# Kernel tuning notes

Hardware: AMD Instinct MI355X
Metric: run time of the kernel (lower is better)

Reference implementation:

```python
import jax, jax.numpy as jnp
import numpy as np

D_MODEL = 1024
NUM_HEADS = 16
D_K = D_MODEL // NUM_HEADS

def setup_inputs() -> dict:
    key = jax.random.key(0)
    ks = jax.random.split(key, 8)
    B, S, D = 2, 2048, D_MODEL
    scale = 1.0 / np.sqrt(D)
    return {
        "X_q": jax.random.normal(ks[0], (B, S, D), dtype=jnp.float32),
        "X_k": jax.random.normal(ks[1], (B, S, D), dtype=jnp.float32),
        "X_v": jax.random.normal(ks[2], (B, S, D), dtype=jnp.float32),
        "W_q": jax.random.normal(ks[3], (D, D), dtype=jnp.float32) * scale,
        "W_k": jax.random.normal(ks[4], (D, D), dtype=jnp.float32) * scale,
        "W_v": jax.random.normal(ks[5], (D, D), dtype=jnp.float32) * scale,
        "W_o": jax.random.normal(ks[6], (D, D), dtype=jnp.float32) * scale,
        "b_o": jnp.zeros((D,), dtype=jnp.float32),
    }

def reference(X_q, X_k, X_v, W_q, W_k, W_v, W_o, b_o):
    B, S, D = X_q.shape
    H, dk = NUM_HEADS, D_K
    # nn.Linear: x @ W.T
    Q = (X_q @ W_q.T).reshape(B, H, S, dk)  # faithful raw view, no transpose
    K = (X_k @ W_k.T).reshape(B, H, S, dk)
    V = (X_v @ W_v.T).reshape(B, H, S, dk)
    A = jnp.einsum("bhqd,bhkd->bhqk", Q, K) / np.sqrt(dk)  # [B,H,S,S]
    A = jax.nn.softmax(A, axis=-1)
    H_cat = jnp.einsum("bhqk,bhkd->bhqd", A, V).reshape(B, S, D)
    return H_cat @ W_o.T + b_o
```

## Files before the change

### kernel.cpp

```cpp
#include <hip/hip_runtime.h>

typedef __bf16 bf16;
typedef bf16 bf16x8 __attribute__((ext_vector_type(8)));
typedef bf16 bf16x4 __attribute__((ext_vector_type(4)));
typedef bf16 bf16x2 __attribute__((ext_vector_type(2)));
typedef float f32x4 __attribute__((ext_vector_type(4)));
typedef float f32x16 __attribute__((ext_vector_type(16)));
typedef int i32x4 __attribute__((ext_vector_type(4)));

#define XSZ 4194304
#define WSZ 1048576
#define KDIM 1024
#define QSCALE 0.1803368801111137f

__device__ __forceinline__ void async16(const bf16* g, bf16* l) {
  __builtin_amdgcn_global_load_lds(
      (const __attribute__((address_space(1))) unsigned int*)g,
      (__attribute__((address_space(3))) unsigned int*)l, 16, 0, 0);
}

__device__ __forceinline__ bf16x8 ld8(const bf16* p) {
  bf16x4 lo = *(const bf16x4*)p;
  bf16x4 hi = *(const bf16x4*)(p + 4);
  return __builtin_shufflevector(lo, hi, 0, 1, 2, 3, 4, 5, 6, 7);
}

__device__ __forceinline__ bf16x8 ld16(const bf16* p) {
  return __builtin_bit_cast(bf16x8, *(const i32x4*)p);
}

__device__ __forceinline__ void st8s(bf16* p, bf16x8 v) {
  *(bf16x4*)p       = __builtin_shufflevector(v, v, 0, 1, 2, 3);
  *(bf16x4*)(p + 4) = __builtin_shufflevector(v, v, 4, 5, 6, 7);
}

__device__ __forceinline__ f32x4 mfma16(bf16x8 a, bf16x8 b, f32x4 c) {
  return __builtin_amdgcn_mfma_f32_16x16x32_bf16(a, b, c, 0, 0, 0);
}
__device__ __forceinline__ f32x16 mfma32(bf16x8 a, bf16x8 b, f32x16 c) {
  return __builtin_amdgcn_mfma_f32_32x32x16_bf16(a, b, c, 0, 0, 0);
}

__device__ __forceinline__ int packbf2(float lo, float hi) {
  bf16x2 t; t[0] = (bf16)lo; t[1] = (bf16)hi;
  return __builtin_bit_cast(int, t);
}

__device__ __forceinline__ float fast_exp2(float x) {
#if __has_builtin(__builtin_amdgcn_exp2f)
  return __builtin_amdgcn_exp2f(x);
#else
  return exp2f(x);
#endif
}


__global__ __launch_bounds__(256) void cast_all(const float* __restrict__ Xq, const float* __restrict__ Xk,
                                                const float* __restrict__ Xv, const float* __restrict__ Wq,
                                                const float* __restrict__ Wk, const float* __restrict__ Wv,
                                                const float* __restrict__ Wo, bf16* __restrict__ dst) {
  size_t i = ((size_t)blockIdx.x * 256 + threadIdx.x) * 8;
  const float* src; size_t off; float scale = 1.0f;
  if (i < XSZ)                { src = Xq; off = i; }
  else if (i < 2 * (size_t)XSZ) { src = Xk; off = i - XSZ; }
  else if (i < 3 * (size_t)XSZ) { src = Xv; off = i - 2 * (size_t)XSZ; }
  else if (i < 3 * (size_t)XSZ + WSZ) { src = Wq; off = i - 3 * (size_t)XSZ; scale = QSCALE; }
  else if (i < 3 * (size_t)XSZ + 2 * (size_t)WSZ) { src = Wk; off = i - 3 * (size_t)XSZ - WSZ; }
  else if (i < 3 * (size_t)XSZ + 3 * (size_t)WSZ) { src = Wv; off = i - 3 * (size_t)XSZ - 2 * (size_t)WSZ; }
  else                        { src = Wo; off = i - 3 * (size_t)XSZ - 3 * (size_t)WSZ; }
  float4 a = *(const float4*)(src + off);
  float4 b = *(const float4*)(src + off + 4);
  bf16x8 o;
  o[0] = (bf16)(a.x * scale); o[1] = (bf16)(a.y * scale);
  o[2] = (bf16)(a.z * scale); o[3] = (bf16)(a.w * scale);
  o[4] = (bf16)(b.x * scale); o[5] = (bf16)(b.y * scale);
  o[6] = (bf16)(b.z * scale); o[7] = (bf16)(b.w * scale);
  *(bf16x8*)(dst + i) = o;
}

__device__ __forceinline__ void gemm_nt_core(const bf16* __restrict__ A, const bf16* __restrict__ Bm,
                                             int m0, int n0, bf16* lds, f32x4 acc[4][4]) {
  const int t = threadIdx.x;
  const int lane = t & 63, wave = t >> 6;
  const int wm = wave & 1, wn = wave >> 1;
  const int quad = lane >> 4, m16 = lane & 15;
  bf16* As = lds;
  bf16* Bs = lds + 128 * 64;
  const bf16* gA[4]; int dstc[4];
  #pragma unroll
  for (int j = 0; j < 4; j++) {
    int c = t + j * 256;
    int row = c >> 3;
    int col = ((c & 7) ^ (row & 7)) * 8;
    gA[j] = A + (size_t)(m0 + row) * KDIM + col;
    dstc[j] = c * 8;
  }
  const ptrdiff_t dBA = (Bm + (size_t)n0 * KDIM) - (A + (size_t)m0 * KDIM);
  const int swz = (m16 & 7) * 8;
  for (int kt = 0; kt < KDIM; kt += 64) {
    #pragma unroll
    for (int j = 0; j < 4; j++) async16(gA[j] + kt, As + dstc[j]);
    #pragma unroll
    for (int j = 0; j < 4; j++) async16(gA[j] + dBA + kt, Bs + dstc[j]);
    __syncthreads();
    #pragma unroll
    for (int s = 0; s < 2; s++) {
      bf16x8 af[4], bfv[4];
      #pragma unroll
      for (int i = 0; i < 4; i++)
        af[i] = ld16(As + (wm * 64 + i * 16 + m16) * 64 + ((s * 32 + quad * 8) ^ swz));
      #pragma unroll
      for (int i = 0; i < 4; i++)
        bfv[i] = ld16(Bs + (wn * 64 + i * 16 + m16) * 64 + ((s * 32 + quad * 8) ^ swz));
      #pragma unroll
      for (int mi = 0; mi < 4; mi++)
        #pragma unroll
        for (int ni = 0; ni < 4; ni++)
          acc[mi][ni] = mfma16(af[mi], bfv[ni], acc[mi][ni]);
    }
    __syncthreads();
  }
}

__global__ __launch_bounds__(256, 3) void proj_gemm(const bf16* __restrict__ xq, const bf16* __restrict__ xk,
                                                 const bf16* __restrict__ xv, const bf16* __restrict__ wq,
                                                 const bf16* __restrict__ wk, const bf16* __restrict__ wv,
                                                 bf16* __restrict__ Qo, bf16* __restrict__ Ko,
                                                 bf16* __restrict__ Vo) {
  __shared__ __align__(16) bf16 lds[2 * 128 * 64];
  const int z = blockIdx.z;
  const bf16* A = (z == 0) ? xq : (z == 1) ? xk : xv;
  const bf16* W = (z == 0) ? wq : (z == 1) ? wk : wv;
  bf16* C = (z == 0) ? Qo : (z == 1) ? Ko : Vo;
  f32x4 acc[4][4];
  #pragma unroll
  for (int i = 0; i < 4; i++)
    #pragma unroll
    for (int j = 0; j < 4; j++) acc[i][j] = (f32x4){0.f, 0.f, 0.f, 0.f};
  gemm_nt_core(A, W, blockIdx.y * 128, blockIdx.x * 128, lds, acc);
  const int lane = threadIdx.x & 63, wave = threadIdx.x >> 6;
  const int wm = wave & 1, wn = wave >> 1, quad = lane >> 4, m16 = lane & 15;
  const int row0 = blockIdx.y * 128 + wm * 64;
  const int col0 = blockIdx.x * 128 + wn * 64;
  #pragma unroll
  for (int mi = 0; mi < 4; mi++)
    #pragma unroll
    for (int ni = 0; ni < 4; ni++)
      #pragma unroll
      for (int r = 0; r < 4; r++) {
        int row = row0 + mi * 16 + quad * 4 + r;
        int col = col0 + ni * 16 + m16;
        C[(size_t)row * 1024 + col] = (bf16)acc[mi][ni][r];
      }
}

__global__ __launch_bounds__(256, 3) void out_gemm(const bf16* __restrict__ Hm, const bf16* __restrict__ wo,
                                                const float* __restrict__ bias, float* __restrict__ out) {
  __shared__ __align__(16) bf16 lds[128 * 64 + 64 * 64];
  bf16* As = lds;
  bf16* Bs = lds + 128 * 64;
  const int t = threadIdx.x;
  const int lane = t & 63, wave = t >> 6;
  const int wm = wave & 1, wn = wave >> 1;
  const int quad = lane >> 4, m16 = lane & 15;
  const int m0 = blockIdx.y * 128, n0 = blockIdx.x * 64;
  const bf16* gA[4]; int dstA[4];
  #pragma unroll
  for (int j = 0; j < 4; j++) {
    int c = t + j * 256;
    int row = c >> 3;
    int col = ((c & 7) ^ (row & 7)) * 8;
    gA[j] = Hm + (size_t)(m0 + row) * KDIM + col;
    dstA[j] = c * 8;
  }
  const bf16* gB[2]; int dstB[2];
  #pragma unroll
  for (int j = 0; j < 2; j++) {
    int c = t + j * 256;
    int row = c >> 3;
    int col = ((c & 7) ^ (row & 7)) * 8;
    gB[j] = wo + (size_t)(n0 + row) * KDIM + col;
    dstB[j] = c * 8;
  }
  const int swz = (m16 & 7) * 8;
  f32x4 acc[4][2];
  #pragma unroll
  for (int i = 0; i < 4; i++)
    #pragma unroll
    for (int j = 0; j < 2; j++) acc[i][j] = (f32x4){0.f, 0.f, 0.f, 0.f};
  for (int kt = 0; kt < KDIM; kt += 64) {
    #pragma unroll
    for (int j = 0; j < 4; j++) async16(gA[j] + kt, As + dstA[j]);
    #pragma unroll
    for (int j = 0; j < 2; j++) async16(gB[j] + kt, Bs + dstB[j]);
    __syncthreads();
    #pragma unroll
    for (int s = 0; s < 2; s++) {
      bf16x8 af[4], bfv[2];
      #pragma unroll
      for (int i = 0; i < 4; i++)
        af[i] = ld16(As + (wm * 64 + i * 16 + m16) * 64 + ((s * 32 + quad * 8) ^ swz));
      #pragma unroll
      for (int i = 0; i < 2; i++)
        bfv[i] = ld16(Bs + (wn * 32 + i * 16 + m16) * 64 + ((s * 32 + quad * 8) ^ swz));
      #pragma unroll
      for (int mi = 0; mi < 4; mi++)
        #pragma unroll
        for (int ni = 0; ni < 2; ni++)
          acc[mi][ni] = mfma16(af[mi], bfv[ni], acc[mi][ni]);
    }
    __syncthreads();
  }
  const int row0 = m0 + wm * 64;
  const int col0 = n0 + wn * 32;
  float bv[2];
  #pragma unroll
  for (int ni = 0; ni < 2; ni++) bv[ni] = bias[col0 + ni * 16 + m16];
  #pragma unroll
  for (int mi = 0; mi < 4; mi++)
    #pragma unroll
    for (int ni = 0; ni < 2; ni++)
      #pragma unroll
      for (int r = 0; r < 4; r++) {
        int row = row0 + mi * 16 + quad * 4 + r;
        int col = col0 + ni * 16 + m16;
        out[(size_t)row * 1024 + col] = acc[mi][ni][r] + bv[ni];
      }
}

__global__ __launch_bounds__(256) void transpose_v(const bf16* __restrict__ V, bf16* __restrict__ Vt) {
  __shared__ bf16 T[64 * 65];
  const int t = threadIdx.x;
  const bf16* src = V + (size_t)blockIdx.y * (2048 * 64) + (size_t)blockIdx.x * 64 * 64;
  bf16* dst = Vt + (size_t)blockIdx.y * (2048 * 64) + (size_t)blockIdx.x * 64;
  #pragma unroll
  for (int j = 0; j < 2; j++) {
    int c = t + j * 256;
    int row = c >> 3, col8 = (c & 7) * 8;
    bf16x8 v = *(const bf16x8*)(src + row * 64 + col8);
    #pragma unroll
    for (int i = 0; i < 8; i++) T[row * 65 + col8 + i] = v[i];
  }
  __syncthreads();
  #pragma unroll
  for (int j = 0; j < 2; j++) {
    int c = t + j * 256;
    int d = c >> 3, k8 = (c & 7) * 8;
    bf16x8 o;
    #pragma unroll
    for (int i = 0; i < 8; i++) o[i] = T[(k8 + i) * 65 + d];
    *(bf16x8*)(dst + (size_t)d * 2048 + k8) = o;
  }
}

#define KS 68
#define VS 132
#define HALF_LDS (128 * KS + 64 * VS)
__global__ __launch_bounds__(512, 2) void attn_kernel(const bf16* __restrict__ Qg,
                                                      const bf16* __restrict__ Kg,
                                                      const bf16* __restrict__ Vtg,
                                                      bf16* __restrict__ Hout) {
  __shared__ bf16 smem[2 * HALF_LDS];
  const int t = threadIdx.x;
  const int lane = t & 63;
  const int w = (t >> 6) & 3;
  const int half = t >> 8;
  const int tt = t & 255;
  const int l31 = lane & 31, h = lane >> 5;
  bf16* Ks = smem + half * HALF_LDS;
  bf16* Vs = Ks + 128 * KS;
  const int L = blockIdx.x + 16 * blockIdx.y;
  const int xcd = L & 7, j5 = L >> 3;
  const int bh = xcd * 4 + (j5 & 3);
  const int qt = j5 >> 2;
  const size_t base = (size_t)bh * (2048 * 64);
  const bf16* Kp = Kg + base;
  const bf16* Vp = Vtg + base;
  const int q = qt * 128 + w * 32 + l31;

  bf16x8 qf[4];
  #pragma unroll
  for (int kc = 0; kc < 4; kc++)
    qf[kc] = *(const bf16x8*)(Qg + base + (size_t)q * 64 + 16 * kc + 8 * h);

  f32x16 oacc[2];
  #pragma unroll
  for (int mt = 0; mt < 2; mt++)
    #pragma unroll
    for (int i = 0; i < 16; i++) oacc[mt][i] = 0.f;
  float lrow = 0.f;

  int krow[4], kcol[4], vrow[4], vcol[4];
  #pragma unroll
  for (int j = 0; j < 4; j++) {
    int c = tt + j * 256;
    krow[j] = c >> 3;  kcol[j] = (c & 7) * 8;
    vrow[j] = c >> 4;  vcol[j] = (c & 15) * 8;
  }

  const int tile0 = half * 8;
  bf16x8 kreg[4], vreg[4];
  #pragma unroll
  for (int j = 0; j < 4; j++) {
    kreg[j] = *(const bf16x8*)(Kp + (size_t)(tile0 * 128 + krow[j]) * 64 + kcol[j]);
    vreg[j] = *(const bf16x8*)(Vp + (size_t)vrow[j] * 2048 + tile0 * 128 + vcol[j]);
  }

  for (int kt = 0; kt < 8; kt++) {
    #pragma unroll
    for (int j = 0; j < 4; j++) st8s(Ks + krow[j] * KS + kcol[j], kreg[j]);
    #pragma unroll
    for (int j = 0; j < 4; j++) st8s(Vs + vrow[j] * VS + vcol[j], vreg[j]);
    __syncthreads();

    if (kt + 1 < 8) {
      const int tg = tile0 + kt + 1;
      #pragma unroll
      for (int j = 0; j < 4; j++) {
        kreg[j] = *(const bf16x8*)(Kp + (size_t)(tg * 128 + krow[j]) * 64 + kcol[j]);
        vreg[j] = *(const bf16x8*)(Vp + (size_t)vrow[j] * 2048 + tg * 128 + vcol[j]);
      }
    }

    #pragma unroll
    for (int mt = 0; mt < 4; mt++) {
      f32x16 sacc;
      #pragma unroll
      for (int i = 0; i < 16; i++) sacc[i] = 0.f;
      #pragma unroll
      for (int kc = 0; kc < 4; kc++) {
        bf16x8 kf = ld8(Ks + (32 * mt + l31) * KS + 16 * kc + 8 * h);
        sacc = mfma32(kf, qf[kc], sacc);
      }
      int pd[8];
      float sum = 0.f;
      #pragma unroll
      for (int p = 0; p < 8; p++) {
        float p0 = fast_exp2(sacc[2 * p]);
        float p1 = fast_exp2(sacc[2 * p + 1]);
        sum += p0 + p1;
        pd[p] = packbf2(p0, p1);
      }
      lrow += sum;
      #pragma unroll
      for (int c1 = 0; c1 < 2; c1++) {
        const int kc = 2 * mt + c1;
        const int rro = 2 * c1 + h;
        const int rrp = 2 * c1 + 1 - h;
        int s0 = __shfl_xor(pd[2 * rrp], 32, 64);
        int s1 = __shfl_xor(pd[2 * rrp + 1], 32, 64);
        int o0 = pd[2 * rro], o1 = pd[2 * rro + 1];
        i32x4 w4;
        w4.x = h ? s0 : o0;
        w4.y = h ? s1 : o1;
        w4.z = h ? o0 : s0;
        w4.w = h ? o1 : s1;
        bf16x8 pfrag = __builtin_bit_cast(bf16x8, w4);
        #pragma unroll
        for (int mtd = 0; mtd < 2; mtd++) {
          bf16x8 vf = ld8(Vs + (32 * mtd + l31) * VS + 16 * kc + 8 * h);
          oacc[mtd] = mfma32(vf, pfrag, oacc[mtd]);
        }
      }
    }
    __syncthreads();
  }

  lrow += __shfl_xor(lrow, 32, 64);
  float* Sf = (float*)smem;
  float* Tf = Sf + w * 2048;
  float* Lb = Sf + 8192 + w * 32;
  if (half) {
    #pragma unroll
    for (int mt = 0; mt < 2; mt++)
      #pragma unroll
      for (int r = 0; r < 16; r++) {
        int d = 32 * mt + (r & 3) + 8 * (r >> 2) + 4 * h;
        Tf[d * 32 + l31] = oacc[mt][r];
      }
    if (!h) Lb[l31] = lrow;
  }
  __syncthreads();
  if (!half) {
    float linv = 1.f / (lrow + Lb[l31]);
    #pragma unroll
    for (int mt = 0; mt < 2; mt++)
      #pragma unroll
      for (int r = 0; r < 16; r++) {
        int d = 32 * mt + (r & 3) + 8 * (r >> 2) + 4 * h;
        Tf[d * 32 + l31] = (oacc[mt][r] + Tf[d * 32 + l31]) * linv;
      }
  }
  __syncthreads();
  bf16* Hq = Hout + base + (size_t)(qt * 128 + w * 32 + l31) * 64 + 32 * h;
  #pragma unroll
  for (int s = 0; s < 2; s++) {
    int se = half * 2 + s;
    bf16x8 o;
    #pragma unroll
    for (int i = 0; i < 8; i++) o[i] = (bf16)Tf[(32 * h + se * 8 + i) * 32 + l31];
    *(bf16x8*)(Hq + se * 8) = o;
  }
}

extern "C" void kernel_launch(void* const* d_in, const int* in_sizes, int n_in,
                              void* d_out, int out_size, void* d_ws, size_t ws_size,
                              hipStream_t stream) {
  const float* Xq = (const float*)d_in[0];
  const float* Xk = (const float*)d_in[1];
  const float* Xv = (const float*)d_in[2];
  const float* Wq = (const float*)d_in[3];
  const float* Wk = (const float*)d_in[4];
  const float* Wv = (const float*)d_in[5];
  const float* Wo = (const float*)d_in[6];
  const float* bo = (const float*)d_in[7];

  bf16* ws = (bf16*)d_ws;
  bf16* xq = ws;
  bf16* xk = ws + XSZ;
  bf16* xv = ws + 2 * (size_t)XSZ;
  bf16* wq = ws + 3 * (size_t)XSZ;
  bf16* wk = wq + WSZ;
  bf16* wv = wk + WSZ;
  bf16* wo = wv + WSZ;
  bf16* q  = wo + WSZ;
  bf16* k  = q + XSZ;
  bf16* v  = k + XSZ;
  bf16* vt = xv;
  bf16* h  = xq;

  cast_all<<<8192, 256, 0, stream>>>(Xq, Xk, Xv, Wq, Wk, Wv, Wo, ws);
  proj_gemm<<<dim3(8, 32, 3), 256, 0, stream>>>(xq, xk, xv, wq, wk, wv, q, k, v);
  transpose_v<<<dim3(32, 32), 256, 0, stream>>>(v, vt);
  attn_kernel<<<dim3(16, 32), 512, 0, stream>>>(q, k, vt, h);
  out_gemm<<<dim3(16, 32), 256, 0, stream>>>(h, wo, bo, (float*)d_out);
}
```

Before: 245.4 us.

## Stream attention K/V tiles with async LDS loads into swizzled double buffers

Replaces the register-staged K/V tile loads, which go through padded LDS rows, with direct global-to-LDS async loads. These fill two ping-pong buffers of 64-key tiles, using an XOR column swizzle in place of padding to avoid bank conflicts. The loop now runs 16 smaller steps with one barrier each, and the next tile's load is issued before the current tile is computed. This removes register pressure and the LDS store instructions, and overlaps global traffic with MFMA work. It relies on the barrier also waiting for the outstanding async loads, and takes more barriers in total because each tile is smaller.

```diff
diff --git a/kernel.cpp b/kernel.cpp
--- a/kernel.cpp
+++ b/kernel.cpp
@@ -19,19 +19,8 @@
       (__attribute__((address_space(3))) unsigned int*)l, 16, 0, 0);
 }
 
-__device__ __forceinline__ bf16x8 ld8(const bf16* p) {
-  bf16x4 lo = *(const bf16x4*)p;
-  bf16x4 hi = *(const bf16x4*)(p + 4);
-  return __builtin_shufflevector(lo, hi, 0, 1, 2, 3, 4, 5, 6, 7);
-}
-
 __device__ __forceinline__ bf16x8 ld16(const bf16* p) {
   return __builtin_bit_cast(bf16x8, *(const i32x4*)p);
-}
-
-__device__ __forceinline__ void st8s(bf16* p, bf16x8 v) {
-  *(bf16x4*)p       = __builtin_shufflevector(v, v, 0, 1, 2, 3);
-  *(bf16x4*)(p + 4) = __builtin_shufflevector(v, v, 4, 5, 6, 7);
 }
 
 __device__ __forceinline__ f32x4 mfma16(bf16x8 a, bf16x8 b, f32x4 c) {
@@ -253,22 +242,18 @@
   }
 }
 
-#define KS 68
-#define VS 132
-#define HALF_LDS (128 * KS + 64 * VS)
 __global__ __launch_bounds__(512, 2) void attn_kernel(const bf16* __restrict__ Qg,
                                                       const bf16* __restrict__ Kg,
                                                       const bf16* __restrict__ Vtg,
                                                       bf16* __restrict__ Hout) {
-  __shared__ bf16 smem[2 * HALF_LDS];
+  __shared__ __align__(16) bf16 smem[32768];
   const int t = threadIdx.x;
   const int lane = t & 63;
   const int w = (t >> 6) & 3;
   const int half = t >> 8;
   const int tt = t & 255;
-  const int l31 = lane & 31, h = lane >> 5;
-  bf16* Ks = smem + half * HALF_LDS;
-  bf16* Vs = Ks + 128 * KS;
+  const int l31 = lane & 31, h = lane >> 5, l7 = lane & 7;
+  bf16* hb = smem + half * 16384;
   const int L = blockIdx.x + 16 * blockIdx.y;
   const int xcd = L & 7, j5 = L >> 3;
   const int bh = xcd * 4 + (j5 & 3);
@@ -290,46 +275,45 @@
     for (int i = 0; i < 16; i++) oacc[mt][i] = 0.f;
   float lrow = 0.f;
 
-  int krow[4], kcol[4], vrow[4], vcol[4];
-  #pragma unroll
-  for (int j = 0; j < 4; j++) {
+  const bf16* ksrc[2]; const bf16* vsrc[2]; int dstc[2];
+  #pragma unroll
+  for (int j = 0; j < 2; j++) {
     int c = tt + j * 256;
-    krow[j] = c >> 3;  kcol[j] = (c & 7) * 8;
-    vrow[j] = c >> 4;  vcol[j] = (c & 15) * 8;
-  }
-
-  const int tile0 = half * 8;
-  bf16x8 kreg[4], vreg[4];
-  #pragma unroll
-  for (int j = 0; j < 4; j++) {
-    kreg[j] = *(const bf16x8*)(Kp + (size_t)(tile0 * 128 + krow[j]) * 64 + kcol[j]);
-    vreg[j] = *(const bf16x8*)(Vp + (size_t)vrow[j] * 2048 + tile0 * 128 + vcol[j]);
-  }
-
-  for (int kt = 0; kt < 8; kt++) {
-    #pragma unroll
-    for (int j = 0; j < 4; j++) st8s(Ks + krow[j] * KS + kcol[j], kreg[j]);
-    #pragma unroll
-    for (int j = 0; j < 4; j++) st8s(Vs + vrow[j] * VS + vcol[j], vreg[j]);
+    int row = c >> 3;
+    int sw = ((c & 7) ^ (row & 7)) * 8;
+    ksrc[j] = Kp + (size_t)(half * 1024 + row) * 64 + sw;
+    vsrc[j] = Vp + (size_t)row * 2048 + half * 1024 + sw;
+    dstc[j] = c * 8;
+  }
+
+  #pragma unroll
+  for (int j = 0; j < 2; j++) {
+    async16(ksrc[j], hb + dstc[j]);
+    async16(vsrc[j], hb + 4096 + dstc[j]);
+  }
+
+  for (int st = 0; st < 16; ++st) {
     __syncthreads();
-
-    if (kt + 1 < 8) {
-      const int tg = tile0 + kt + 1;
-      #pragma unroll
-      for (int j = 0; j < 4; j++) {
-        kreg[j] = *(const bf16x8*)(Kp + (size_t)(tg * 128 + krow[j]) * 64 + kcol[j]);
-        vreg[j] = *(const bf16x8*)(Vp + (size_t)vrow[j] * 2048 + tg * 128 + vcol[j]);
+    const int buf = st & 1;
+    if (st + 1 < 16) {
+      const int nb = (buf ^ 1) * 8192;
+      #pragma unroll
+      for (int j = 0; j < 2; j++) {
+        async16(ksrc[j] + (st + 1) * 4096, hb + nb + dstc[j]);
+        async16(vsrc[j] + (st + 1) * 64,   hb + nb + 4096 + dstc[j]);
       }
     }
-
-    #pragma unroll
-    for (int mt = 0; mt < 4; mt++) {
+    bf16* Kb = hb + buf * 8192;
+    bf16* Vb = Kb + 4096;
+
+    #pragma unroll
+    for (int mtq = 0; mtq < 2; mtq++) {
       f32x16 sacc;
       #pragma unroll
       for (int i = 0; i < 16; i++) sacc[i] = 0.f;
       #pragma unroll
       for (int kc = 0; kc < 4; kc++) {
-        bf16x8 kf = ld8(Ks + (32 * mt + l31) * KS + 16 * kc + 8 * h);
+        bf16x8 kf = ld16(Kb + (32 * mtq + l31) * 64 + (((2 * kc + h) ^ l7) << 3));
         sacc = mfma32(kf, qf[kc], sacc);
       }
       int pd[8];
@@ -344,7 +328,7 @@
       lrow += sum;
       #pragma unroll
       for (int c1 = 0; c1 < 2; c1++) {
-        const int kc = 2 * mt + c1;
+        const int kcp = 2 * mtq + c1;
         const int rro = 2 * c1 + h;
         const int rrp = 2 * c1 + 1 - h;
         int s0 = __shfl_xor(pd[2 * rrp], 32, 64);
@@ -358,13 +342,13 @@
         bf16x8 pfrag = __builtin_bit_cast(bf16x8, w4);
         #pragma unroll
         for (int mtd = 0; mtd < 2; mtd++) {
-          bf16x8 vf = ld8(Vs + (32 * mtd + l31) * VS + 16 * kc + 8 * h);
+          bf16x8 vf = ld16(Vb + (32 * mtd + l31) * 64 + (((2 * kcp + h) ^ l7) << 3));
           oacc[mtd] = mfma32(vf, pfrag, oacc[mtd]);
         }
       }
     }
-    __syncthreads();
-  }
+  }
+  __syncthreads();
 
   lrow += __shfl_xor(lrow, 32, 64);
   float* Sf = (float*)smem;
```

Result: faster. 238.3 us (-2.9%).
